# Optimization experiments

Hardware: AMD Instinct MI355X
Metric: run time of the kernel (lower is better)

Reference implementation:

```python
import jax, jax.numpy as jnp
import numpy as np

EPS = 1e-5
DIM = 128
SCALE = DIM ** (-0.5)


def setup_inputs() -> dict:
    key = jax.random.key(0)
    k1, k2, k3 = jax.random.split(key, 3)
    B, N, D = 2, 128 * 128, DIM
    Q = N // 4
    x = jax.random.normal(k1, (B, N, D), dtype=jnp.float32)
    gamma = jnp.ones((D,), dtype=jnp.float32)
    beta = jnp.zeros((D,), dtype=jnp.float32)
    queries = jax.random.normal(k2, (Q, D), dtype=jnp.float32)
    W = jax.random.normal(k3, (2 * D, D), dtype=jnp.float32) * (1.0 / np.sqrt(D))
    return {"x": x, "gamma": gamma, "beta": beta, "queries": queries, "W": W}


def reference(x, gamma, beta, queries, W):
    # LayerNorm over last dim (eps matches torch default 1e-5)
    mu = jnp.mean(x, axis=-1, keepdims=True)
    var = jnp.mean(jnp.square(x - mu), axis=-1, keepdims=True)
    xn = (x - mu) * jax.lax.rsqrt(var + EPS) * gamma + beta  # [B, N, D]
    # learned-query cross attention: sim = Q @ xn^T * scale -> softmax -> @ xn
    sim = jnp.einsum('qd,bnd->bqn', queries, xn) * SCALE     # [B, Q, N]
    attn = jax.nn.softmax(sim, axis=-1)
    out = jnp.einsum('bqn,bnd->bqd', attn, xn)               # [B, Q, D]
    # trailing linear: dim -> 2*dim, no bias
    return jnp.einsum('bqd,ed->bqe', out, W)                 # [B, Q, 2D]
```

## Files before the change

### kernel.cpp

```cpp
#include <hip/hip_runtime.h>
#include <stdint.h>

#define Nn 16384
#define Dd 128
#define Qq 4096
#define Ee 256
#define KV 64

typedef __bf16 bf16x8 __attribute__((ext_vector_type(8)));
typedef float floatx16 __attribute__((ext_vector_type(16)));
typedef unsigned uintx2 __attribute__((ext_vector_type(2)));

__device__ __forceinline__ float fexp2(float x) {
#if __has_builtin(__builtin_amdgcn_exp2f)
  return __builtin_amdgcn_exp2f(x);
#else
  return exp2f(x);
#endif
}
__device__ __forceinline__ unsigned pk_bf(float lo, float hi) {
  return __builtin_amdgcn_perm(__float_as_uint(hi) + 0x8000u,
                               __float_as_uint(lo) + 0x8000u, 0x07060302u);
}
__device__ __forceinline__ void stage16(const void* g, void* lds_uniform) {
  __builtin_amdgcn_global_load_lds(
      (const __attribute__((address_space(1))) unsigned int*)g,
      (__attribute__((address_space(3))) unsigned int*)lds_uniform, 16, 0, 0);
}
__device__ __forceinline__ void plswap(unsigned a, unsigned b, int hi,
                                       unsigned& r0, unsigned& r1) {
#if __has_builtin(__builtin_amdgcn_permlane32_swap)
  uintx2 r = __builtin_amdgcn_permlane32_swap(a, b, false, false);
  r0 = r[0];
  r1 = r[1];
  (void)hi;
#else
  unsigned ax = __shfl_xor(a, 32);
  unsigned bx = __shfl_xor(b, 32);
  r0 = hi ? bx : a;
  r1 = hi ? b : ax;
#endif
}

__global__ __launch_bounds__(256) void k_lnt(
    const float* __restrict__ x, const float* __restrict__ gamma,
    const float* __restrict__ beta, const float* __restrict__ queries,
    const float* __restrict__ W, unsigned* __restrict__ xn,
    unsigned short* __restrict__ xnT, unsigned short* __restrict__ qb,
    unsigned short* __restrict__ wb) {
  __shared__ __align__(16) uint2 lds2[64 * 32];
  const int tid = threadIdx.x;
  const int bid = blockIdx.x;
  const int b = bid >> 8, n0 = (bid & 255) * 64;
  const int r = tid >> 2, qd = tid & 3;

  const float4* xp = (const float4*)(x + ((size_t)(b * Nn + n0 + r)) * Dd + qd * 32);
  float4 v[8];
  float s = 0.f, s2 = 0.f;
#pragma unroll
  for (int i = 0; i < 8; ++i) {
    v[i] = xp[i];
    s += (v[i].x + v[i].y) + (v[i].z + v[i].w);
    s2 += (v[i].x * v[i].x + v[i].y * v[i].y) + (v[i].z * v[i].z + v[i].w * v[i].w);
  }
  s += __shfl_xor(s, 1); s2 += __shfl_xor(s2, 1);
  s += __shfl_xor(s, 2); s2 += __shfl_xor(s2, 2);
  float mu = s * (1.0f / 128.0f);
  float var = s2 * (1.0f / 128.0f) - mu * mu;
  float rs = rsqrtf(var + 1e-5f);

  const float4* gp = (const float4*)(gamma + qd * 32);
  const float4* bp = (const float4*)(beta + qd * 32);
  unsigned pk[16];
#pragma unroll
  for (int i = 0; i < 8; ++i) {
    float4 g = gp[i], bt = bp[i];
    pk[2 * i] = pk_bf((v[i].x - mu) * rs * g.x + bt.x, (v[i].y - mu) * rs * g.y + bt.y);
    pk[2 * i + 1] = pk_bf((v[i].z - mu) * rs * g.z + bt.z, (v[i].w - mu) * rs * g.w + bt.w);
  }
  unsigned* xrow = xn + ((size_t)(b * Nn + n0 + r)) * 64;
#pragma unroll
  for (int j = 0; j < 4; ++j)
    *(uint4*)(xrow + (((qd * 4 + j) ^ (r & 7)) * 4)) =
        make_uint4(pk[4 * j], pk[4 * j + 1], pk[4 * j + 2], pk[4 * j + 3]);
  const int rk = r & 31;
#pragma unroll
  for (int kk = 0; kk < 8; ++kk)
    lds2[r * 32 + ((qd * 8 + kk) ^ rk)] = make_uint2(pk[2 * kk], pk[2 * kk + 1]);
  __syncthreads();
  const int dq = tid >> 3, nc = tid & 7;
  uint2 U[8];
#pragma unroll
  for (int j = 0; j < 8; ++j) {
    int rr = nc * 8 + j;
    U[j] = lds2[rr * 32 + (dq ^ (rr & 31))];
  }
#pragma unroll
  for (int e = 0; e < 4; ++e) {
    int d = dq * 4 + e;
    unsigned a0 = (e & 2) ? U[0].y : U[0].x, a1 = (e & 2) ? U[1].y : U[1].x;
    unsigned a2 = (e & 2) ? U[2].y : U[2].x, a3 = (e & 2) ? U[3].y : U[3].x;
    unsigned a4 = (e & 2) ? U[4].y : U[4].x, a5 = (e & 2) ? U[5].y : U[5].x;
    unsigned a6 = (e & 2) ? U[6].y : U[6].x, a7 = (e & 2) ? U[7].y : U[7].x;
    unsigned sel = (e & 1) ? 0x07060302u : 0x05040100u;
    uint4 o;
    o.x = __builtin_amdgcn_perm(a1, a0, sel);
    o.y = __builtin_amdgcn_perm(a3, a2, sel);
    o.z = __builtin_amdgcn_perm(a5, a4, sel);
    o.w = __builtin_amdgcn_perm(a7, a6, sel);
    *(uint4*)(xnT + ((size_t)(b * Dd + d)) * Nn + n0 + (nc ^ (d & 7)) * 8) = o;
  }
  const float QSC = 0.08838834764831845f * 1.4426950408889634f;
  const int total4 = (Qq * Dd + Ee * Dd) / 4;
  for (int u = bid * 256 + tid; u < total4; u += 512 * 256) {
    if (u < Qq * Dd / 4) {
      float4 v4 = ((const float4*)queries)[u];
      ((uint2*)qb)[u] = make_uint2(pk_bf(v4.x * QSC, v4.y * QSC),
                                   pk_bf(v4.z * QSC, v4.w * QSC));
    } else {
      float4 v4 = ((const float4*)W)[u - Qq * Dd / 4];
      ((uint2*)wb)[u - Qq * Dd / 4] =
          make_uint2(pk_bf(v4.x, v4.y), pk_bf(v4.z, v4.w));
    }
  }
}

template <int NS, int NWAVE>
__global__ __launch_bounds__(NWAVE * 64, 2) void k_attn(
    const unsigned short* __restrict__ xn,
    const unsigned short* __restrict__ xnT,
    const unsigned short* __restrict__ qb,
    float* __restrict__ o_part,
    float* __restrict__ l_part) {
  constexpr int NCH = Nn / NS;
  constexpr int NIT = NCH / KV;
  constexpr int QT = Qq / (32 * NWAVE);
  constexpr int CPW = 16 / NWAVE;
  __shared__ __align__(16) char lds_x[2][16384];
  __shared__ __align__(16) char lds_xt[3][16384];

  const int bid = blockIdx.x;
  const int split = bid % NS;
  const int qt = (bid / NS) % QT;
  const int b = bid / (NS * QT);
  const int tid = threadIdx.x;
  const int wave = tid >> 6, lane = tid & 63;
  const int col = lane & 31, half = lane >> 5;
  const int ck = col & 7;
  const int qwbase = qt * (32 * NWAVE) + wave * 32;

  bf16x8 qf[8];
#pragma unroll
  for (int s = 0; s < 8; ++s)
    qf[s] = *(const bf16x8*)(qb + (size_t)(qwbase + col) * Dd + s * 16 + half * 8);

  const floatx16 fz = {0.f,0.f,0.f,0.f,0.f,0.f,0.f,0.f,0.f,0.f,0.f,0.f,0.f,0.f,0.f,0.f};
  floatx16 O[4];
#pragma unroll
  for (int d = 0; d < 4; ++d) O[d] = fz;
  float lsum = 0.f;

  const char* gx = (const char*)xn + (size_t)b * Nn * 256;
  const char* gxt = (const char*)xnT + (size_t)b * Dd * Nn * 2;
  const int tbase = split * NCH / KV;

  auto stgX = [&](int t, int buf) {
    const char* xsrc = gx + (size_t)(tbase + t) * (KV * 256);
#pragma unroll
    for (int p = 0; p < CPW; ++p) {
      int m = wave * CPW + p;
      stage16(xsrc + m * 1024 + lane * 16, &lds_x[buf][0] + m * 1024);
    }
  };
  auto stgXT = [&](int t, int buf) {
#pragma unroll
    for (int p = 0; p < CPW; ++p) {
      int m = wave * CPW + p;
      const char* g = gxt + (size_t)(m * 8 + (lane >> 3)) * (Nn * 2) +
                      (size_t)(tbase + t) * (KV * 2) + (lane & 7) * 16;
      stage16(g, &lds_xt[buf][0] + m * 1024);
    }
  };
  auto sphase = [&](const char* lx, floatx16* S) {
#pragma unroll
    for (int s = 0; s < 8; ++s)
#pragma unroll
      for (int mt = 0; mt < 2; ++mt) {
        bf16x8 ax = *(const bf16x8*)(lx + (32 * mt + col) * 256 +
                                     (((2 * s + half) ^ ck) * 16));
        S[mt] = __builtin_amdgcn_mfma_f32_32x32x16_bf16(ax, qf[s], S[mt], 0, 0, 0);
      }
  };
  auto expphase = [&](const floatx16* S, unsigned P[2][4][2]) {
#pragma unroll
    for (int mt = 0; mt < 2; ++mt)
#pragma unroll
      for (int t = 0; t < 4; ++t) {
        float p0 = fexp2(S[mt][4 * t]);
        float p1 = fexp2(S[mt][4 * t + 1]);
        float p2 = fexp2(S[mt][4 * t + 2]);
        float p3 = fexp2(S[mt][4 * t + 3]);
        lsum += (p0 + p1) + (p2 + p3);
        P[mt][t][0] = pk_bf(p0, p1);
        P[mt][t][1] = pk_bf(p2, p3);
      }
  };
  auto pvphase = [&](const char* lxt, unsigned P[2][4][2]) {
#pragma unroll
    for (int s2 = 0; s2 < 4; ++s2) {
      const int mt = s2 >> 1, ge = 2 * (s2 & 1), go = ge + 1;
      unsigned w0, w1, w2, w3;
      plswap(P[mt][ge][0], P[mt][go][0], half, w0, w2);
      plswap(P[mt][ge][1], P[mt][go][1], half, w1, w3);
      union { uint4 u; bf16x8 v; } ap;
      ap.u = make_uint4(w0, w1, w2, w3);
#pragma unroll
      for (int dn = 0; dn < 4; ++dn) {
        bf16x8 bx = *(const bf16x8*)(lxt + (32 * dn + col) * 128 +
                                     (((2 * s2 + half) ^ ck) * 16));
        O[dn] = __builtin_amdgcn_mfma_f32_32x32x16_bf16(ap.v, bx, O[dn], 0, 0, 0);
      }
    }
  };

  stgX(0, 0); stgXT(0, 0);
  stgX(1, 1); stgXT(1, 1);
  asm volatile("s_waitcnt vmcnt(8)" ::: "memory");
  __builtin_amdgcn_s_barrier();
  __builtin_amdgcn_sched_barrier(0);

  unsigned P[2][4][2];
  {
    floatx16 S[2]; S[0] = fz; S[1] = fz;
    __builtin_amdgcn_s_setprio(1);
    sphase(&lds_x[0][0], S);
    __builtin_amdgcn_s_setprio(0);
    expphase(S, P);
  }
  asm volatile("" ::: "memory");
  __builtin_amdgcn_s_barrier();
  if (NIT > 2) { stgX(2, 0); stgXT(2, 2); }

  int xtc = 0;
#pragma unroll 1
  for (int i = 1; i < NIT; ++i) {
    if (i + 1 < NIT) {
      asm volatile("s_waitcnt vmcnt(8)" ::: "memory");
    } else {
      asm volatile("s_waitcnt vmcnt(0)" ::: "memory");
    }
    __builtin_amdgcn_s_barrier();
    __builtin_amdgcn_sched_barrier(0);

    const char* lx = &lds_x[i & 1][0];
    const char* lxt = &lds_xt[xtc][0];

    floatx16 S[2]; S[0] = fz; S[1] = fz;
    __builtin_amdgcn_s_setprio(1);
    sphase(lx, S);
    pvphase(lxt, P);
    __builtin_amdgcn_s_setprio(0);
    expphase(S, P);

    asm volatile("" ::: "memory");
    __builtin_amdgcn_s_barrier();
    if (i + 2 < NIT) { stgX(i + 2, i & 1); stgXT(i + 2, xtc); }
    xtc = (xtc == 2) ? 0 : xtc + 1;
  }
  pvphase(&lds_xt[xtc][0], P);

  float lt = lsum + __shfl_xor(lsum, 32);
  if (half == 0)
    l_part[(size_t)(b * NS + split) * Qq + qwbase + col] = lt;
  float* op = o_part + ((size_t)(b * NS + split) * Qq + qwbase) * Dd;
#pragma unroll
  for (int dn = 0; dn < 4; ++dn)
#pragma unroll
    for (int r = 0; r < 16; ++r) {
      int q = (r & 3) + 8 * (r >> 2) + 4 * half;
      op[(size_t)q * Dd + dn * 32 + col] = O[dn][r];
    }
}

template <int NS>
__global__ __launch_bounds__(256) void k_comb(
    const float* __restrict__ o_part, const float* __restrict__ l_part,
    const unsigned short* __restrict__ wb, float* __restrict__ out) {
  __shared__ __align__(16) char lds_a[32 * 256];
  __shared__ float lds_linv[32];
  const int bid = blockIdx.x;
  const int b = bid >> 7, qc = bid & 127;
  const int qbase = qc * 32;
  const int tid = threadIdx.x;
  const int wave = tid >> 6, lane = tid & 63;
  const int col = lane & 31, half = lane >> 5;
  const int ck = col & 7;

  if (tid < 32) {
    float l = 0.f;
#pragma unroll
    for (int s = 0; s < NS; ++s)
      l += l_part[(size_t)(b * NS + s) * Qq + qbase + tid];
    lds_linv[tid] = 1.0f / l;
  }
  __syncthreads();

#pragma unroll
  for (int i = 0; i < 4; ++i) {
    int idx = i * 256 + tid;
    int q = idx >> 5, d4 = idx & 31;
    float4 acc = make_float4(0.f, 0.f, 0.f, 0.f);
#pragma unroll
    for (int s = 0; s < NS; ++s) {
      float4 v = *(const float4*)(o_part + ((size_t)(b * NS + s) * Qq + qbase + q) * Dd + d4 * 4);
      acc.x += v.x; acc.y += v.y; acc.z += v.z; acc.w += v.w;
    }
    float li = lds_linv[q];
    int w = d4 >> 1;
    int pos = (w & 8) | ((w ^ (q & 7)) & 7);
    *(uint2*)(lds_a + q * 256 + pos * 16 + (d4 & 1) * 8) =
        make_uint2(pk_bf(acc.x * li, acc.y * li), pk_bf(acc.z * li, acc.w * li));
  }
  __syncthreads();

  bf16x8 af[8];
#pragma unroll
  for (int s = 0; s < 8; ++s) {
    int u = 2 * s + half;
    int pos = (u & 8) | ((u ^ ck) & 7);
    af[s] = *(const bf16x8*)(lds_a + col * 256 + pos * 16);
  }

  const floatx16 fz = {0.f,0.f,0.f,0.f,0.f,0.f,0.f,0.f,0.f,0.f,0.f,0.f,0.f,0.f,0.f,0.f};
#pragma unroll
  for (int et = 0; et < 2; ++et) {
    floatx16 C = fz;
    int e_row = wave * 64 + et * 32 + col;
#pragma unroll
    for (int s = 0; s < 8; ++s) {
      bf16x8 bw = *(const bf16x8*)(wb + (size_t)e_row * Dd + s * 16 + half * 8);
      C = __builtin_amdgcn_mfma_f32_32x32x16_bf16(af[s], bw, C, 0, 0, 0);
    }
#pragma unroll
    for (int r = 0; r < 16; ++r) {
      int q = qbase + (r & 3) + 8 * (r >> 2) + 4 * half;
      out[((size_t)b * Qq + q) * Ee + wave * 64 + et * 32 + col] = C[r];
    }
  }
}

extern "C" void kernel_launch(void* const* d_in, const int* in_sizes, int n_in,
                              void* d_out, int out_size, void* d_ws, size_t ws_size,
                              hipStream_t stream) {
  const float* x = (const float*)d_in[0];
  const float* gamma = (const float*)d_in[1];
  const float* beta = (const float*)d_in[2];
  const float* queries = (const float*)d_in[3];
  const float* W = (const float*)d_in[4];
  float* out = (float*)d_out;

  char* w = (char*)d_ws;
  unsigned short* xn = (unsigned short*)(w);
  unsigned short* xnT = (unsigned short*)(w + 8388608);
  unsigned short* qb = (unsigned short*)(w + 16777216);
  unsigned short* wb = (unsigned short*)(w + 17825792);
  float* o_part = (float*)(w + 17891328);
  float* l_part = (float*)(w + 51445760);

  k_lnt<<<dim3(512), dim3(256), 0, stream>>>(x, gamma, beta, queries, W,
                                             (unsigned*)xn, xnT, qb, wb);
  k_attn<8, 4><<<dim3(512), dim3(256), 0, stream>>>(xn, xnT, qb, o_part, l_part);
  k_comb<8><<<dim3(256), dim3(256), 0, stream>>>(o_part, l_part, wb, out);
}
```

Measured before the change: 158.7 us.

## Fuse three kernels into one cooperative launch with grid syncs

Merges the layernorm/transpose, attention and combine kernels into a single cooperative kernel separated by grid-wide syncs, with a fallback to the three separate launches if the cooperative launch fails. The goal is to remove the launch gaps and tail drain between kernels. In exchange, the combine stage leaves half the blocks idle, every block now holds 80KB of shared memory, and grid sync adds its own overhead.

```diff
diff --git a/kernel.cpp b/kernel.cpp
--- a/kernel.cpp
+++ b/kernel.cpp
@@ -1,11 +1,19 @@
 #include <hip/hip_runtime.h>
+#include <hip/hip_cooperative_groups.h>
 #include <stdint.h>
+
+namespace cg = cooperative_groups;
 
 #define Nn 16384
 #define Dd 128
 #define Qq 4096
 #define Ee 256
 #define KV 64
+#define NS 8
+#define NWAVE 4
+#define NIT 32
+#define QT 32
+#define CPW 4
 
 typedef __bf16 bf16x8 __attribute__((ext_vector_type(8)));
 typedef float floatx16 __attribute__((ext_vector_type(16)));
@@ -42,15 +50,12 @@
 #endif
 }
 
-__global__ __launch_bounds__(256) void k_lnt(
-    const float* __restrict__ x, const float* __restrict__ gamma,
-    const float* __restrict__ beta, const float* __restrict__ queries,
-    const float* __restrict__ W, unsigned* __restrict__ xn,
-    unsigned short* __restrict__ xnT, unsigned short* __restrict__ qb,
-    unsigned short* __restrict__ wb) {
-  __shared__ __align__(16) uint2 lds2[64 * 32];
-  const int tid = threadIdx.x;
-  const int bid = blockIdx.x;
+__device__ __forceinline__ void lnt_body(
+    int bid, int tid, char* smem,
+    const float* x, const float* gamma, const float* beta,
+    const float* queries, const float* W, unsigned* xn,
+    unsigned short* xnT, unsigned short* qb, unsigned short* wb) {
+  uint2* lds2 = (uint2*)smem;
   const int b = bid >> 8, n0 = (bid & 255) * 64;
   const int r = tid >> 2, qd = tid & 3;
 
@@ -125,29 +130,18 @@
   }
 }
 
-template <int NS, int NWAVE>
-__global__ __launch_bounds__(NWAVE * 64, 2) void k_attn(
-    const unsigned short* __restrict__ xn,
-    const unsigned short* __restrict__ xnT,
-    const unsigned short* __restrict__ qb,
-    float* __restrict__ o_part,
-    float* __restrict__ l_part) {
-  constexpr int NCH = Nn / NS;
-  constexpr int NIT = NCH / KV;
-  constexpr int QT = Qq / (32 * NWAVE);
-  constexpr int CPW = 16 / NWAVE;
-  __shared__ __align__(16) char lds_x[2][16384];
-  __shared__ __align__(16) char lds_xt[3][16384];
-
-  const int bid = blockIdx.x;
+__device__ __forceinline__ void attn_body(
+    int bid, int tid, char* smem,
+    const unsigned short* xn, const unsigned short* xnT,
+    const unsigned short* qb, float* o_part, float* l_part) {
   const int split = bid % NS;
   const int qt = (bid / NS) % QT;
   const int b = bid / (NS * QT);
-  const int tid = threadIdx.x;
   const int wave = tid >> 6, lane = tid & 63;
   const int col = lane & 31, half = lane >> 5;
   const int ck = col & 7;
   const int qwbase = qt * (32 * NWAVE) + wave * 32;
+  char* lxt0 = smem + 32768;
 
   bf16x8 qf[8];
 #pragma unroll
@@ -162,14 +156,14 @@
 
   const char* gx = (const char*)xn + (size_t)b * Nn * 256;
   const char* gxt = (const char*)xnT + (size_t)b * Dd * Nn * 2;
-  const int tbase = split * NCH / KV;
+  const int tbase = split * (NIT);
 
   auto stgX = [&](int t, int buf) {
     const char* xsrc = gx + (size_t)(tbase + t) * (KV * 256);
 #pragma unroll
     for (int p = 0; p < CPW; ++p) {
       int m = wave * CPW + p;
-      stage16(xsrc + m * 1024 + lane * 16, &lds_x[buf][0] + m * 1024);
+      stage16(xsrc + m * 1024 + lane * 16, smem + (buf << 14) + m * 1024);
     }
   };
   auto stgXT = [&](int t, int buf) {
@@ -178,7 +172,7 @@
       int m = wave * CPW + p;
       const char* g = gxt + (size_t)(m * 8 + (lane >> 3)) * (Nn * 2) +
                       (size_t)(tbase + t) * (KV * 2) + (lane & 7) * 16;
-      stage16(g, &lds_xt[buf][0] + m * 1024);
+      stage16(g, lxt0 + (buf << 14) + m * 1024);
     }
   };
   auto sphase = [&](const char* lx, floatx16* S) {
@@ -233,7 +227,7 @@
   {
     floatx16 S[2]; S[0] = fz; S[1] = fz;
     __builtin_amdgcn_s_setprio(1);
-    sphase(&lds_x[0][0], S);
+    sphase(smem, S);
     __builtin_amdgcn_s_setprio(0);
     expphase(S, P);
   }
@@ -252,8 +246,8 @@
     __builtin_amdgcn_s_barrier();
     __builtin_amdgcn_sched_barrier(0);
 
-    const char* lx = &lds_x[i & 1][0];
-    const char* lxt = &lds_xt[xtc][0];
+    const char* lx = smem + ((i & 1) << 14);
+    const char* lxt = lxt0 + (xtc << 14);
 
     floatx16 S[2]; S[0] = fz; S[1] = fz;
     __builtin_amdgcn_s_setprio(1);
@@ -267,7 +261,7 @@
     if (i + 2 < NIT) { stgX(i + 2, i & 1); stgXT(i + 2, xtc); }
     xtc = (xtc == 2) ? 0 : xtc + 1;
   }
-  pvphase(&lds_xt[xtc][0], P);
+  pvphase(lxt0 + (xtc << 14), P);
 
   float lt = lsum + __shfl_xor(lsum, 32);
   if (half == 0)
@@ -282,16 +276,14 @@
     }
 }
 
-template <int NS>
-__global__ __launch_bounds__(256) void k_comb(
-    const float* __restrict__ o_part, const float* __restrict__ l_part,
-    const unsigned short* __restrict__ wb, float* __restrict__ out) {
-  __shared__ __align__(16) char lds_a[32 * 256];
-  __shared__ float lds_linv[32];
-  const int bid = blockIdx.x;
+__device__ __forceinline__ void comb_body(
+    int bid, int tid, char* smem,
+    const float* o_part, const float* l_part,
+    const unsigned short* wb, float* out) {
+  char* lds_a = smem;
+  float* lds_linv = (float*)(smem + 8192);
   const int b = bid >> 7, qc = bid & 127;
   const int qbase = qc * 32;
-  const int tid = threadIdx.x;
   const int wave = tid >> 6, lane = tid & 63;
   const int col = lane & 31, half = lane >> 5;
   const int ck = col & 7;
@@ -347,6 +339,50 @@
       out[((size_t)b * Qq + q) * Ee + wave * 64 + et * 32 + col] = C[r];
     }
   }
+}
+
+__global__ __launch_bounds__(256, 2) void k_fused(
+    const float* __restrict__ x, const float* __restrict__ gamma,
+    const float* __restrict__ beta, const float* __restrict__ queries,
+    const float* __restrict__ W, unsigned* xn, unsigned short* xnT,
+    unsigned short* qb, unsigned short* wb, float* o_part, float* l_part,
+    float* out) {
+  __shared__ __align__(16) char smem[81920];
+  const int bid = blockIdx.x, tid = threadIdx.x;
+
+  lnt_body(bid, tid, smem, x, gamma, beta, queries, W, xn, xnT, qb, wb);
+  __syncthreads();
+  __threadfence();
+  cg::this_grid().sync();
+
+  attn_body(bid, tid, smem, (const unsigned short*)xn, xnT, qb, o_part, l_part);
+  __syncthreads();
+  __threadfence();
+  cg::this_grid().sync();
+
+  if (bid < 256)
+    comb_body(bid, tid, smem, o_part, l_part, wb, out);
+}
+
+__global__ __launch_bounds__(256) void k_lnt(
+    const float* __restrict__ x, const float* __restrict__ gamma,
+    const float* __restrict__ beta, const float* __restrict__ queries,
+    const float* __restrict__ W, unsigned* xn, unsigned short* xnT,
+    unsigned short* qb, unsigned short* wb) {
+  __shared__ __align__(16) char smem[16384];
+  lnt_body(blockIdx.x, threadIdx.x, smem, x, gamma, beta, queries, W, xn, xnT, qb, wb);
+}
+__global__ __launch_bounds__(256, 2) void k_attn(
+    const unsigned short* __restrict__ xn, const unsigned short* __restrict__ xnT,
+    const unsigned short* __restrict__ qb, float* o_part, float* l_part) {
+  __shared__ __align__(16) char smem[81920];
+  attn_body(blockIdx.x, threadIdx.x, smem, xn, xnT, qb, o_part, l_part);
+}
+__global__ __launch_bounds__(256) void k_comb(
+    const float* __restrict__ o_part, const float* __restrict__ l_part,
+    const unsigned short* __restrict__ wb, float* out) {
+  __shared__ __align__(16) char smem[8320];
+  comb_body(blockIdx.x, threadIdx.x, smem, o_part, l_part, wb, out);
 }
 
 extern "C" void kernel_launch(void* const* d_in, const int* in_sizes, int n_in,
@@ -360,15 +396,24 @@
   float* out = (float*)d_out;
 
   char* w = (char*)d_ws;
-  unsigned short* xn = (unsigned short*)(w);
+  unsigned* xn = (unsigned*)(w);
   unsigned short* xnT = (unsigned short*)(w + 8388608);
   unsigned short* qb = (unsigned short*)(w + 16777216);
   unsigned short* wb = (unsigned short*)(w + 17825792);
   float* o_part = (float*)(w + 17891328);
   float* l_part = (float*)(w + 51445760);
 
-  k_lnt<<<dim3(512), dim3(256), 0, stream>>>(x, gamma, beta, queries, W,
-                                             (unsigned*)xn, xnT, qb, wb);
-  k_attn<8, 4><<<dim3(512), dim3(256), 0, stream>>>(xn, xnT, qb, o_part, l_part);
-  k_comb<8><<<dim3(256), dim3(256), 0, stream>>>(o_part, l_part, wb, out);
-}
+  void* args[12] = {(void*)&x,  (void*)&gamma, (void*)&beta, (void*)&queries,
+                    (void*)&W,  (void*)&xn,    (void*)&xnT,  (void*)&qb,
+                    (void*)&wb, (void*)&o_part, (void*)&l_part, (void*)&out};
+  hipError_t e = hipLaunchCooperativeKernel((const void*)k_fused, dim3(512),
+                                            dim3(256), args, 0, stream);
+  if (e != hipSuccess) {
+    (void)hipGetLastError();
+    k_lnt<<<dim3(512), dim3(256), 0, stream>>>(x, gamma, beta, queries, W,
+                                               xn, xnT, qb, wb);
+    k_attn<<<dim3(512), dim3(256), 0, stream>>>((const unsigned short*)xn, xnT,
+                                                qb, o_part, l_part);
+    k_comb<<<dim3(256), dim3(256), 0, stream>>>(o_part, l_part, wb, out);
+  }
+}
```

Result: slower. 392.2 us (+147.1%).

## Interleave per-tile QK, PV and exp work with ping-pong P buffers

Applied to the files above, without the earlier changes.

Restructures the attention main loop so each 32-row half of the QK^T tile is computed, then half of the previous tile's PV MFMAs are issued, then that half's exp is done. This interleaves MFMA and transcendental/VALU work at finer grain, and uses two P register buffers (unrolled by two) instead of one. The aim is better overlap of exp with matrix-core work, at the cost of more live registers and possible occupancy pressure. The tbase expression and pointer cast changes are cosmetic.

```diff
diff --git a/kernel.cpp b/kernel.cpp
--- a/kernel.cpp
+++ b/kernel.cpp
@@ -162,7 +162,7 @@
 
   const char* gx = (const char*)xn + (size_t)b * Nn * 256;
   const char* gxt = (const char*)xnT + (size_t)b * Dd * Nn * 2;
-  const int tbase = split * NCH / KV;
+  const int tbase = split * (NCH / KV);
 
   auto stgX = [&](int t, int buf) {
     const char* xsrc = gx + (size_t)(tbase + t) * (KV * 256);
@@ -181,46 +181,78 @@
       stage16(g, &lds_xt[buf][0] + m * 1024);
     }
   };
-  auto sphase = [&](const char* lx, floatx16* S) {
+  auto sread = [&](const char* lx, int mt, int s) {
+    return *(const bf16x8*)(lx + (32 * mt + col) * 256 +
+                            (((2 * s + half) ^ ck) * 16));
+  };
+  auto exp_mt = [&](const floatx16& S, unsigned Pm[4][2]) {
+#pragma unroll
+    for (int t = 0; t < 4; ++t) {
+      float p0 = fexp2(S[4 * t]);
+      float p1 = fexp2(S[4 * t + 1]);
+      float p2 = fexp2(S[4 * t + 2]);
+      float p3 = fexp2(S[4 * t + 3]);
+      lsum += (p0 + p1) + (p2 + p3);
+      Pm[t][0] = pk_bf(p0, p1);
+      Pm[t][1] = pk_bf(p2, p3);
+    }
+  };
+  auto pv_s2 = [&](const char* lxt, unsigned (&P)[2][4][2], int s2) {
+    const int mt = s2 >> 1, ge = 2 * (s2 & 1), go = ge + 1;
+    unsigned w0, w1, w2, w3;
+    plswap(P[mt][ge][0], P[mt][go][0], half, w0, w2);
+    plswap(P[mt][ge][1], P[mt][go][1], half, w1, w3);
+    union { uint4 u; bf16x8 v; } ap;
+    ap.u = make_uint4(w0, w1, w2, w3);
+#pragma unroll
+    for (int dn = 0; dn < 4; ++dn) {
+      bf16x8 bx = *(const bf16x8*)(lxt + (32 * dn + col) * 128 +
+                                   (((2 * s2 + half) ^ ck) * 16));
+      O[dn] = __builtin_amdgcn_mfma_f32_32x32x16_bf16(ap.v, bx, O[dn], 0, 0, 0);
+    }
+  };
+
+  int xt_prev = 0;
+
+  auto body = [&](int i, unsigned (&Pprev)[2][4][2], unsigned (&Pcur)[2][4][2]) {
+    if (i + 1 < NIT) {
+      asm volatile("s_waitcnt vmcnt(8)" ::: "memory");
+    } else {
+      asm volatile("s_waitcnt vmcnt(0)" ::: "memory");
+    }
+    __builtin_amdgcn_s_barrier();
+    __builtin_amdgcn_sched_barrier(0);
+
+    const char* lx = &lds_x[i & 1][0];
+    const char* lxt = &lds_xt[xt_prev][0];
+
+    floatx16 S0 = fz;
+    __builtin_amdgcn_s_setprio(1);
 #pragma unroll
     for (int s = 0; s < 8; ++s)
-#pragma unroll
-      for (int mt = 0; mt < 2; ++mt) {
-        bf16x8 ax = *(const bf16x8*)(lx + (32 * mt + col) * 256 +
-                                     (((2 * s + half) ^ ck) * 16));
-        S[mt] = __builtin_amdgcn_mfma_f32_32x32x16_bf16(ax, qf[s], S[mt], 0, 0, 0);
-      }
-  };
-  auto expphase = [&](const floatx16* S, unsigned P[2][4][2]) {
-#pragma unroll
-    for (int mt = 0; mt < 2; ++mt)
-#pragma unroll
-      for (int t = 0; t < 4; ++t) {
-        float p0 = fexp2(S[mt][4 * t]);
-        float p1 = fexp2(S[mt][4 * t + 1]);
-        float p2 = fexp2(S[mt][4 * t + 2]);
-        float p3 = fexp2(S[mt][4 * t + 3]);
-        lsum += (p0 + p1) + (p2 + p3);
-        P[mt][t][0] = pk_bf(p0, p1);
-        P[mt][t][1] = pk_bf(p2, p3);
-      }
-  };
-  auto pvphase = [&](const char* lxt, unsigned P[2][4][2]) {
-#pragma unroll
-    for (int s2 = 0; s2 < 4; ++s2) {
-      const int mt = s2 >> 1, ge = 2 * (s2 & 1), go = ge + 1;
-      unsigned w0, w1, w2, w3;
-      plswap(P[mt][ge][0], P[mt][go][0], half, w0, w2);
-      plswap(P[mt][ge][1], P[mt][go][1], half, w1, w3);
-      union { uint4 u; bf16x8 v; } ap;
-      ap.u = make_uint4(w0, w1, w2, w3);
-#pragma unroll
-      for (int dn = 0; dn < 4; ++dn) {
-        bf16x8 bx = *(const bf16x8*)(lxt + (32 * dn + col) * 128 +
-                                     (((2 * s2 + half) ^ ck) * 16));
-        O[dn] = __builtin_amdgcn_mfma_f32_32x32x16_bf16(ap.v, bx, O[dn], 0, 0, 0);
-      }
-    }
+      S0 = __builtin_amdgcn_mfma_f32_32x32x16_bf16(sread(lx, 0, s), qf[s], S0, 0, 0, 0);
+    pv_s2(lxt, Pprev, 0);
+    pv_s2(lxt, Pprev, 1);
+    __builtin_amdgcn_s_setprio(0);
+    exp_mt(S0, Pcur[0]);
+
+    floatx16 S1 = fz;
+    __builtin_amdgcn_s_setprio(1);
+#pragma unroll
+    for (int s = 0; s < 8; ++s)
+      S1 = __builtin_amdgcn_mfma_f32_32x32x16_bf16(sread(lx, 1, s), qf[s], S1, 0, 0, 0);
+    pv_s2(lxt, Pprev, 2);
+    pv_s2(lxt, Pprev, 3);
+    __builtin_amdgcn_s_setprio(0);
+    exp_mt(S1, Pcur[1]);
+
+    asm volatile("" ::: "memory");
+    __builtin_amdgcn_s_barrier();
+    if (i + 2 < NIT) {
+      stgX(i + 2, i & 1);
+      stgXT(i + 2, xt_prev);
+    }
+    xt_prev = (xt_prev == 2) ? 0 : xt_prev + 1;
   };
 
   stgX(0, 0); stgXT(0, 0);
@@ -229,45 +261,34 @@
   __builtin_amdgcn_s_barrier();
   __builtin_amdgcn_sched_barrier(0);
 
-  unsigned P[2][4][2];
+  unsigned PA[2][4][2], PB[2][4][2];
   {
-    floatx16 S[2]; S[0] = fz; S[1] = fz;
+    floatx16 S0 = fz, S1 = fz;
     __builtin_amdgcn_s_setprio(1);
-    sphase(&lds_x[0][0], S);
+#pragma unroll
+    for (int s = 0; s < 8; ++s)
+      S0 = __builtin_amdgcn_mfma_f32_32x32x16_bf16(sread(&lds_x[0][0], 0, s), qf[s], S0, 0, 0, 0);
+#pragma unroll
+    for (int s = 0; s < 8; ++s)
+      S1 = __builtin_amdgcn_mfma_f32_32x32x16_bf16(sread(&lds_x[0][0], 1, s), qf[s], S1, 0, 0, 0);
     __builtin_amdgcn_s_setprio(0);
-    expphase(S, P);
+    exp_mt(S0, PA[0]);
+    exp_mt(S1, PA[1]);
   }
   asm volatile("" ::: "memory");
   __builtin_amdgcn_s_barrier();
   if (NIT > 2) { stgX(2, 0); stgXT(2, 2); }
 
-  int xtc = 0;
 #pragma unroll 1
-  for (int i = 1; i < NIT; ++i) {
-    if (i + 1 < NIT) {
-      asm volatile("s_waitcnt vmcnt(8)" ::: "memory");
-    } else {
-      asm volatile("s_waitcnt vmcnt(0)" ::: "memory");
-    }
-    __builtin_amdgcn_s_barrier();
-    __builtin_amdgcn_sched_barrier(0);
-
-    const char* lx = &lds_x[i & 1][0];
-    const char* lxt = &lds_xt[xtc][0];
-
-    floatx16 S[2]; S[0] = fz; S[1] = fz;
-    __builtin_amdgcn_s_setprio(1);
-    sphase(lx, S);
-    pvphase(lxt, P);
-    __builtin_amdgcn_s_setprio(0);
-    expphase(S, P);
-
-    asm volatile("" ::: "memory");
-    __builtin_amdgcn_s_barrier();
-    if (i + 2 < NIT) { stgX(i + 2, i & 1); stgXT(i + 2, xtc); }
-    xtc = (xtc == 2) ? 0 : xtc + 1;
-  }
-  pvphase(&lds_xt[xtc][0], P);
+  for (int i = 1; i + 1 < NIT; i += 2) {
+    body(i, PA, PB);
+    body(i + 1, PB, PA);
+  }
+  body(NIT - 1, PA, PB);
+  pv_s2(&lds_xt[xt_prev][0], PB, 0);
+  pv_s2(&lds_xt[xt_prev][0], PB, 1);
+  pv_s2(&lds_xt[xt_prev][0], PB, 2);
+  pv_s2(&lds_xt[xt_prev][0], PB, 3);
 
   float lt = lsum + __shfl_xor(lsum, 32);
   if (half == 0)
@@ -360,7 +381,7 @@
   float* out = (float*)d_out;
 
   char* w = (char*)d_ws;
-  unsigned short* xn = (unsigned short*)(w);
+  unsigned* xn = (unsigned*)(w);
   unsigned short* xnT = (unsigned short*)(w + 8388608);
   unsigned short* qb = (unsigned short*)(w + 16777216);
   unsigned short* wb = (unsigned short*)(w + 17825792);
@@ -368,7 +389,8 @@
   float* l_part = (float*)(w + 51445760);
 
   k_lnt<<<dim3(512), dim3(256), 0, stream>>>(x, gamma, beta, queries, W,
-                                             (unsigned*)xn, xnT, qb, wb);
-  k_attn<8, 4><<<dim3(512), dim3(256), 0, stream>>>(xn, xnT, qb, o_part, l_part);
+                                             xn, xnT, qb, wb);
+  k_attn<8, 4><<<dim3(512), dim3(256), 0, stream>>>((const unsigned short*)xn,
+                                                    xnT, qb, o_part, l_part);
   k_comb<8><<<dim3(256), dim3(256), 0, stream>>>(o_part, l_part, wb, out);
 }
```

Result: no change. 159.7 us (+0.6%).
